# Kernel tuning notes

Hardware: AMD Instinct MI355X
Metric: run time of the kernel (lower is better)

Reference implementation:

```python
import jax, jax.numpy as jnp
import numpy as np

B, S, SIZE = 2048, 512, 96  # size = embedding_size(32) * num_feature(3)


def setup_inputs() -> dict:
    key = jax.random.key(0)
    k1, k2, k3, k4, k5, k6, k7 = jax.random.split(key, 7)
    bound = 1.0 / np.sqrt(SIZE)  # nn.Linear default init range
    return {
        "seq_item_embedding": jax.random.normal(k1, (B, S, SIZE), dtype=jnp.float32),
        "target_item_embedding": jax.random.normal(k2, (B, 1, SIZE), dtype=jnp.float32),
        "mask": jax.random.randint(k3, (B, S + 1, 1), 0, 2).astype(jnp.bool_),
        "w1_weight": jax.random.uniform(k4, (SIZE, SIZE), jnp.float32, -bound, bound),
        "w1_bias": jax.random.uniform(k5, (SIZE,), jnp.float32, -bound, bound),
        "w2_weight": jax.random.uniform(k6, (SIZE, SIZE), jnp.float32, -bound, bound),
        "w2_bias": jax.random.uniform(k7, (SIZE,), jnp.float32, -bound, bound),
    }


def reference(seq_item_embedding, target_item_embedding, mask,
              w1_weight, w1_bias, w2_weight, w2_bias):
    # mask[:, :-1, :] -> [B, S] boolean (True = masked out)
    m = mask[:, :-1, 0]
    # w1(seq): [B, S, size]; note source reassigns seq_item_embedding to this,
    # so the final weighted pool uses the projected sequence.
    seq_h = jnp.einsum('bsd,ed->bse', seq_item_embedding, w1_weight) + w1_bias
    # w2(target): [B, 1, size], broadcasts over seq_len (repeat in torch)
    tgt_h = jnp.einsum('bqd,ed->bqe', target_item_embedding, w2_weight) + w2_bias
    # sigmoid(sum) reduced over feature dim -> scores [B, S]
    scores = jax.nn.sigmoid(seq_h + tgt_h).sum(axis=-1)
    scores = jnp.where(m, jnp.float32(-1e9), scores)
    attn = jax.nn.softmax(scores, axis=-1)  # [B, S]
    # weighted pool over seq dim -> [B, size]
    output = jnp.einsum('bs,bse->be', attn, seq_h)
    return output
```

## Files before the change

kernel.cpp:

```cpp
#include <hip/hip_runtime.h>
#include <math.h>

#define NB 2048
#define NS 512
#define ND 96

typedef __attribute__((ext_vector_type(8))) short short8;
typedef __attribute__((ext_vector_type(4))) float floatx4;

__device__ __forceinline__ unsigned f2bfu(float f) {
    union { float f; unsigned u; } c; c.f = f;
    unsigned u = c.u;
    u += 0x7FFF + ((u >> 16) & 1);
    return u >> 16;
}
__device__ __forceinline__ float sigm(float x) {
    return 1.0f / (1.0f + __expf(-x));
}
__device__ __forceinline__ short8 cvt8(floatx4 p0, floatx4 p1) {
    short8 v;
    v[0]=(short)f2bfu(p0[0]); v[1]=(short)f2bfu(p0[1]);
    v[2]=(short)f2bfu(p0[2]); v[3]=(short)f2bfu(p0[3]);
    v[4]=(short)f2bfu(p1[0]); v[5]=(short)f2bfu(p1[1]);
    v[6]=(short)f2bfu(p1[2]); v[7]=(short)f2bfu(p1[3]);
    return v;
}

__global__ __launch_bounds__(512, 2)
void attn_fused(const float* __restrict__ seq,
                const float* __restrict__ tgt,
                const int*   __restrict__ mask,
                const float* __restrict__ w1,
                const float* __restrict__ b1,
                const float* __restrict__ w2,
                const float* __restrict__ b2,
                float* __restrict__ out)
{
    __shared__ short w1f[18 * 64 * 8];
    __shared__ floatx4 thp4[ND];
    __shared__ float maskf[NS];
    __shared__ float red2[8];
    __shared__ float osum[8][ND];

    const int b    = blockIdx.x;
    const int tid  = threadIdx.x;
    const int lane = tid & 63;
    const int wave = tid >> 6;
    const int l15  = lane & 15;
    const int quad = lane >> 4;

    maskf[tid] = (mask[(size_t)b * (NS + 1) + tid] != 0) ? 0.0f : 1.0f;

    for (int idx = tid; idx < 1152; idx += 512) {
        const int e  = idx / 12;
        const int dc = idx - 12 * e;
        const int kk = dc >> 2;
        const int q  = dc & 3;
        const float* p = w1 + e * ND + kk * 32 + q * 8;
        floatx4 p0 = *(const floatx4*)(p);
        floatx4 p1 = *(const floatx4*)(p + 4);
        const int t = e >> 4, r = e & 15;
        *(short8*)&w1f[(((t * 3 + kk) * 64) + q * 16 + r) * 8] = cvt8(p0, p1);
    }

    if (tid < 4 * ND) {
        const int e    = tid >> 2;
        const int part = tid & 3;
        const float* tv = tgt + (size_t)b * ND + part * 24;
        const float* wr = w2 + e * ND + part * 24;
        float acc = 0.f;
        #pragma unroll
        for (int d = 0; d < 24; d += 4) {
            floatx4 a = *(const floatx4*)(tv + d);
            floatx4 w = *(const floatx4*)(wr + d);
            acc += a[0]*w[0] + a[1]*w[1] + a[2]*w[2] + a[3]*w[3];
        }
        thp4[e][part] = acc;
    }
    __syncthreads();

    float tgtv[6], biasv[6];
    #pragma unroll
    for (int t = 0; t < 6; ++t) {
        const int e = 16 * t + l15;
        floatx4 tp = thp4[e];
        tgtv[t]  = b2[e] + tp[0] + tp[1] + tp[2] + tp[3];
        biasv[t] = b1[e];
    }

    const float* abase = seq + ((size_t)b * NS + l15) * ND + quad * 8;
    float o_acc[6] = {0.f, 0.f, 0.f, 0.f, 0.f, 0.f};
    float sacc = 0.f;

    #pragma unroll
    for (int sti = 0; sti < 4; ++sti) {
        const int s0 = (wave * 4 + sti) * 16;
        short8 af[3];
        #pragma unroll
        for (int kk = 0; kk < 3; ++kk) {
            const float* p = abase + (size_t)s0 * ND + kk * 32;
            af[kk] = cvt8(*(const floatx4*)(p), *(const floatx4*)(p + 4));
        }
        floatx4 acc6[6];
        float p0s = 0.f, p1s = 0.f, p2s = 0.f, p3s = 0.f;
        #pragma unroll
        for (int t = 0; t < 6; ++t) {
            floatx4 acc = { biasv[t], biasv[t], biasv[t], biasv[t] };
            #pragma unroll
            for (int kk = 0; kk < 3; ++kk) {
                const short8 bf = *(const short8*)&w1f[((t * 3 + kk) * 64 + lane) * 8];
                acc = __builtin_amdgcn_mfma_f32_16x16x32_bf16(af[kk], bf, acc, 0, 0, 0);
            }
            acc6[t] = acc;
            const float thv = tgtv[t];
            p0s += sigm(acc[0] + thv);
            p1s += sigm(acc[1] + thv);
            p2s += sigm(acc[2] + thv);
            p3s += sigm(acc[3] + thv);
        }
        #pragma unroll
        for (int off = 1; off < 16; off <<= 1) {
            p0s += __shfl_xor(p0s, off, 64);
            p1s += __shfl_xor(p1s, off, 64);
            p2s += __shfl_xor(p2s, off, 64);
            p3s += __shfl_xor(p3s, off, 64);
        }
        const int sq = s0 + quad * 4;
        const float e0 = maskf[sq + 0] * __expf(p0s - 48.f);
        const float e1 = maskf[sq + 1] * __expf(p1s - 48.f);
        const float e2 = maskf[sq + 2] * __expf(p2s - 48.f);
        const float e3 = maskf[sq + 3] * __expf(p3s - 48.f);
        sacc += e0 + e1 + e2 + e3;
        #pragma unroll
        for (int t = 0; t < 6; ++t) {
            o_acc[t] += e0 * acc6[t][0] + e1 * acc6[t][1]
                      + e2 * acc6[t][2] + e3 * acc6[t][3];
        }
    }

    float ss = sacc;
    ss += __shfl_xor(ss, 16, 64);
    ss += __shfl_xor(ss, 32, 64);
    if (lane == 0) red2[wave] = ss;
    __syncthreads();
    float tot = red2[0];
    #pragma unroll
    for (int w = 1; w < 8; ++w) tot += red2[w];

    #pragma unroll
    for (int t = 0; t < 6; ++t) {
        o_acc[t] += __shfl_xor(o_acc[t], 16, 64);
        o_acc[t] += __shfl_xor(o_acc[t], 32, 64);
    }
    if (quad == 0) {
        #pragma unroll
        for (int t = 0; t < 6; ++t) osum[wave][16 * t + l15] = o_acc[t];
    }
    __syncthreads();
    if (tid < ND) {
        float a = 0.f;
        #pragma unroll
        for (int w = 0; w < 8; ++w) a += osum[w][tid];
        out[(size_t)b * ND + tid] = a * (1.0f / tot);
    }
}

extern "C" void kernel_launch(void* const* d_in, const int* in_sizes, int n_in,
                              void* d_out, int out_size, void* d_ws, size_t ws_size,
                              hipStream_t stream) {
    const float* seq  = (const float*)d_in[0];
    const float* tgt  = (const float*)d_in[1];
    const int*   mask = (const int*)d_in[2];
    const float* w1   = (const float*)d_in[3];
    const float* b1   = (const float*)d_in[4];
    const float* w2   = (const float*)d_in[5];
    const float* b2   = (const float*)d_in[6];
    float* out = (float*)d_out;
    attn_fused<<<dim3(NB), dim3(512), 0, stream>>>(seq, tgt, mask, w1, b1, w2, b2, out);
}
```

Measured before the change: 603.5 us.

## Prefetch next sequence tile and use hardware bf16 pack conversion

Issues the global loads for each wave's first sequence tile before the weight staging and target projection, then prefetches the next tile while the current one is processed, so load latency overlaps with compute. It also replaces the manual round-to-nearest-even float-to-bf16 bit manipulation with the packed v_cvt_pk_bf16_f32 instruction via inline asm. The prefetch raises register pressure under launch bounds of 512 threads and 2 blocks, and the asm conversion's rounding behaviour may differ slightly from the manual routine.

```diff
diff --git a/kernel.cpp b/kernel.cpp
--- a/kernel.cpp
+++ b/kernel.cpp
@@ -8,22 +8,16 @@
 typedef __attribute__((ext_vector_type(8))) short short8;
 typedef __attribute__((ext_vector_type(4))) float floatx4;
 
-__device__ __forceinline__ unsigned f2bfu(float f) {
-    union { float f; unsigned u; } c; c.f = f;
-    unsigned u = c.u;
-    u += 0x7FFF + ((u >> 16) & 1);
-    return u >> 16;
-}
 __device__ __forceinline__ float sigm(float x) {
     return 1.0f / (1.0f + __expf(-x));
 }
 __device__ __forceinline__ short8 cvt8(floatx4 p0, floatx4 p1) {
-    short8 v;
-    v[0]=(short)f2bfu(p0[0]); v[1]=(short)f2bfu(p0[1]);
-    v[2]=(short)f2bfu(p0[2]); v[3]=(short)f2bfu(p0[3]);
-    v[4]=(short)f2bfu(p1[0]); v[5]=(short)f2bfu(p1[1]);
-    v[6]=(short)f2bfu(p1[2]); v[7]=(short)f2bfu(p1[3]);
-    return v;
+    union { unsigned u[4]; short8 s; } r;
+    asm("v_cvt_pk_bf16_f32 %0, %1, %2" : "=v"(r.u[0]) : "v"(p0[0]), "v"(p0[1]));
+    asm("v_cvt_pk_bf16_f32 %0, %1, %2" : "=v"(r.u[1]) : "v"(p0[2]), "v"(p0[3]));
+    asm("v_cvt_pk_bf16_f32 %0, %1, %2" : "=v"(r.u[2]) : "v"(p1[0]), "v"(p1[1]));
+    asm("v_cvt_pk_bf16_f32 %0, %1, %2" : "=v"(r.u[3]) : "v"(p1[2]), "v"(p1[3]));
+    return r.s;
 }
 
 __global__ __launch_bounds__(512, 2)
@@ -50,6 +44,17 @@
     const int quad = lane >> 4;
 
     maskf[tid] = (mask[(size_t)b * (NS + 1) + tid] != 0) ? 0.0f : 1.0f;
+
+    const float* abase = seq + ((size_t)b * NS + l15) * ND + quad * 8;
+    floatx4 pre[6];
+    {
+        const float* p = abase + (size_t)(wave * 64) * ND;
+        #pragma unroll
+        for (int kk = 0; kk < 3; ++kk) {
+            pre[2 * kk]     = *(const floatx4*)(p + kk * 32);
+            pre[2 * kk + 1] = *(const floatx4*)(p + kk * 32 + 4);
+        }
+    }
 
     for (int idx = tid; idx < 1152; idx += 512) {
         const int e  = idx / 12;
@@ -88,7 +93,6 @@
         biasv[t] = b1[e];
     }
 
-    const float* abase = seq + ((size_t)b * NS + l15) * ND + quad * 8;
     float o_acc[6] = {0.f, 0.f, 0.f, 0.f, 0.f, 0.f};
     float sacc = 0.f;
 
@@ -96,10 +100,16 @@
     for (int sti = 0; sti < 4; ++sti) {
         const int s0 = (wave * 4 + sti) * 16;
         short8 af[3];
-        #pragma unroll
-        for (int kk = 0; kk < 3; ++kk) {
-            const float* p = abase + (size_t)s0 * ND + kk * 32;
-            af[kk] = cvt8(*(const floatx4*)(p), *(const floatx4*)(p + 4));
+        af[0] = cvt8(pre[0], pre[1]);
+        af[1] = cvt8(pre[2], pre[3]);
+        af[2] = cvt8(pre[4], pre[5]);
+        if (sti < 3) {
+            const float* p = abase + (size_t)(s0 + 16) * ND;
+            #pragma unroll
+            for (int kk = 0; kk < 3; ++kk) {
+                pre[2 * kk]     = *(const floatx4*)(p + kk * 32);
+                pre[2 * kk + 1] = *(const floatx4*)(p + kk * 32 + 4);
+            }
         }
         floatx4 acc6[6];
         float p0s = 0.f, p1s = 0.f, p2s = 0.f, p3s = 0.f;
```

Result: no change. 595.4 us (-1.3%).

## Halve block size to 256 threads, use hardware bf16 pack conversion, drop a barrier

Applied to the files above, without the earlier changes.

Each block now runs 4 waves, and each wave processes 8 sequence tiles (unrolled by 2) instead of 4, with launch bounds changed to 256 threads and 4 blocks per CU. The software round-to-nearest float-to-bf16 conversion is replaced by inline v_cvt_pk_bf16_f32 instructions. The separate sync for the softmax denominator is merged into the final barrier. The aim is lower per-block setup overhead and cheaper conversions, at the cost of more serial work per wave and more per-block staging of W1 into LDS across the grid.

```diff
diff --git a/kernel.cpp b/kernel.cpp
--- a/kernel.cpp
+++ b/kernel.cpp
@@ -8,25 +8,19 @@
 typedef __attribute__((ext_vector_type(8))) short short8;
 typedef __attribute__((ext_vector_type(4))) float floatx4;
 
-__device__ __forceinline__ unsigned f2bfu(float f) {
-    union { float f; unsigned u; } c; c.f = f;
-    unsigned u = c.u;
-    u += 0x7FFF + ((u >> 16) & 1);
-    return u >> 16;
-}
 __device__ __forceinline__ float sigm(float x) {
     return 1.0f / (1.0f + __expf(-x));
 }
 __device__ __forceinline__ short8 cvt8(floatx4 p0, floatx4 p1) {
-    short8 v;
-    v[0]=(short)f2bfu(p0[0]); v[1]=(short)f2bfu(p0[1]);
-    v[2]=(short)f2bfu(p0[2]); v[3]=(short)f2bfu(p0[3]);
-    v[4]=(short)f2bfu(p1[0]); v[5]=(short)f2bfu(p1[1]);
-    v[6]=(short)f2bfu(p1[2]); v[7]=(short)f2bfu(p1[3]);
-    return v;
+    union { unsigned u[4]; short8 s; } r;
+    asm("v_cvt_pk_bf16_f32 %0, %1, %2" : "=v"(r.u[0]) : "v"(p0[0]), "v"(p0[1]));
+    asm("v_cvt_pk_bf16_f32 %0, %1, %2" : "=v"(r.u[1]) : "v"(p0[2]), "v"(p0[3]));
+    asm("v_cvt_pk_bf16_f32 %0, %1, %2" : "=v"(r.u[2]) : "v"(p1[0]), "v"(p1[1]));
+    asm("v_cvt_pk_bf16_f32 %0, %1, %2" : "=v"(r.u[3]) : "v"(p1[2]), "v"(p1[3]));
+    return r.s;
 }
 
-__global__ __launch_bounds__(512, 2)
+__global__ __launch_bounds__(256, 4)
 void attn_fused(const float* __restrict__ seq,
                 const float* __restrict__ tgt,
                 const int*   __restrict__ mask,
@@ -37,10 +31,10 @@
                 float* __restrict__ out)
 {
     __shared__ short w1f[18 * 64 * 8];
-    __shared__ floatx4 thp4[ND];
+    __shared__ float thp2[ND][2];
     __shared__ float maskf[NS];
-    __shared__ float red2[8];
-    __shared__ float osum[8][ND];
+    __shared__ float red2[4];
+    __shared__ float osum[4][ND];
 
     const int b    = blockIdx.x;
     const int tid  = threadIdx.x;
@@ -49,9 +43,10 @@
     const int l15  = lane & 15;
     const int quad = lane >> 4;
 
-    maskf[tid] = (mask[(size_t)b * (NS + 1) + tid] != 0) ? 0.0f : 1.0f;
+    maskf[tid]       = (mask[(size_t)b * (NS + 1) + tid]       != 0) ? 0.0f : 1.0f;
+    maskf[tid + 256] = (mask[(size_t)b * (NS + 1) + tid + 256] != 0) ? 0.0f : 1.0f;
 
-    for (int idx = tid; idx < 1152; idx += 512) {
+    for (int idx = tid; idx < 1152; idx += 256) {
         const int e  = idx / 12;
         const int dc = idx - 12 * e;
         const int kk = dc >> 2;
@@ -63,19 +58,19 @@
         *(short8*)&w1f[(((t * 3 + kk) * 64) + q * 16 + r) * 8] = cvt8(p0, p1);
     }
 
-    if (tid < 4 * ND) {
-        const int e    = tid >> 2;
-        const int part = tid & 3;
-        const float* tv = tgt + (size_t)b * ND + part * 24;
-        const float* wr = w2 + e * ND + part * 24;
+    if (tid < 2 * ND) {
+        const int e    = tid >> 1;
+        const int part = tid & 1;
+        const float* tv = tgt + (size_t)b * ND + part * 48;
+        const float* wr = w2 + e * ND + part * 48;
         float acc = 0.f;
         #pragma unroll
-        for (int d = 0; d < 24; d += 4) {
+        for (int d = 0; d < 48; d += 4) {
             floatx4 a = *(const floatx4*)(tv + d);
             floatx4 w = *(const floatx4*)(wr + d);
             acc += a[0]*w[0] + a[1]*w[1] + a[2]*w[2] + a[3]*w[3];
         }
-        thp4[e][part] = acc;
+        thp2[e][part] = acc;
     }
     __syncthreads();
 
@@ -83,8 +78,7 @@
     #pragma unroll
     for (int t = 0; t < 6; ++t) {
         const int e = 16 * t + l15;
-        floatx4 tp = thp4[e];
-        tgtv[t]  = b2[e] + tp[0] + tp[1] + tp[2] + tp[3];
+        tgtv[t]  = b2[e] + thp2[e][0] + thp2[e][1];
         biasv[t] = b1[e];
     }
 
@@ -92,9 +86,9 @@
     float o_acc[6] = {0.f, 0.f, 0.f, 0.f, 0.f, 0.f};
     float sacc = 0.f;
 
-    #pragma unroll
-    for (int sti = 0; sti < 4; ++sti) {
-        const int s0 = (wave * 4 + sti) * 16;
+    #pragma unroll 2
+    for (int sti = 0; sti < 8; ++sti) {
+        const int s0 = (wave * 8 + sti) * 16;
         short8 af[3];
         #pragma unroll
         for (int kk = 0; kk < 3; ++kk) {
@@ -142,10 +136,6 @@
     ss += __shfl_xor(ss, 16, 64);
     ss += __shfl_xor(ss, 32, 64);
     if (lane == 0) red2[wave] = ss;
-    __syncthreads();
-    float tot = red2[0];
-    #pragma unroll
-    for (int w = 1; w < 8; ++w) tot += red2[w];
 
     #pragma unroll
     for (int t = 0; t < 6; ++t) {
@@ -158,9 +148,10 @@
     }
     __syncthreads();
     if (tid < ND) {
+        const float tot = red2[0] + red2[1] + red2[2] + red2[3];
         float a = 0.f;
         #pragma unroll
-        for (int w = 0; w < 8; ++w) a += osum[w][tid];
+        for (int w = 0; w < 4; ++w) a += osum[w][tid];
         out[(size_t)b * ND + tid] = a * (1.0f / tot);
     }
 }
@@ -176,5 +167,5 @@
     const float* w2   = (const float*)d_in[5];
     const float* b2   = (const float*)d_in[6];
     float* out = (float*)d_out;
-    attn_fused<<<dim3(NB), dim3(512), 0, stream>>>(seq, tgt, mask, w1, b1, w2, b2, out);
+    attn_fused<<<dim3(NB), dim3(256), 0, stream>>>(seq, tgt, mask, w1, b1, w2, b2, out);
 }
```

Result: faster. 583.6 us (-3.3%).
